# Kernel optimization log

Hardware: AMD Instinct MI355X
Metric: run time of the kernel (lower is better)

Reference implementation:

```python
import jax, jax.numpy as jnp
import numpy as np

DIM = 192
NUM_HEADS = 6
KSZ = 7
MLP_RATIO = 4.0
LEVELS = 8
EPS = 1e-5


def layernorm(x, w, b):
    mu = jnp.mean(x, axis=-1, keepdims=True)
    var = jnp.mean(jnp.square(x - mu), axis=-1, keepdims=True)
    return (x - mu) * jax.lax.rsqrt(var + EPS) * w + b


def na2d(x, qkv_w, qkv_b, proj_w, proj_b, rpb):
    # Neighborhood attention 2D with relative position bias (NATTEN semantics:
    # window of KSZ x KSZ keys per query, clamped to stay inside the image).
    B, H, W, C = x.shape
    nh, hd = NUM_HEADS, C // NUM_HEADS
    scale = hd ** -0.5
    qkv = (x @ qkv_w.T + qkv_b).reshape(B, H, W, 3, nh, hd)
    q = qkv[..., 0, :, :] * scale  # [B,H,W,nh,hd]
    k = qkv[..., 1, :, :]
    v = qkv[..., 2, :, :]

    si = jnp.clip(jnp.arange(H) - KSZ // 2, 0, H - KSZ)
    idx_i = si[:, None] + jnp.arange(KSZ)  # [H,KSZ] row indices of each window
    sj = jnp.clip(jnp.arange(W) - KSZ // 2, 0, W - KSZ)
    idx_j = sj[:, None] + jnp.arange(KSZ)  # [W,KSZ]

    def gather_win(t):  # [B,H,W,nh,hd] -> [B,H,KSZ,W,KSZ,nh,hd]
        t = jnp.take(t, idx_i.reshape(-1), axis=1).reshape(B, H, KSZ, W, nh, hd)
        t = jnp.take(t, idx_j.reshape(-1), axis=3).reshape(B, H, KSZ, W, KSZ, nh, hd)
        return t

    kw = gather_win(k)
    vw = gather_win(v)

    # scores over the KSZ x KSZ neighborhood
    scores = jnp.einsum('bxynd,bxiyjnd->bxynij', q, kw)  # [B,H,W,nh,KSZ,KSZ]

    # relative position bias: rpb is [nh, 2K-1, 2K-1]
    rel_i = idx_i - jnp.arange(H)[:, None] + (KSZ - 1)  # [H,KSZ] in [0,2K-2]
    rel_j = idx_j - jnp.arange(W)[:, None] + (KSZ - 1)  # [W,KSZ]
    bias = rpb[:, rel_i][:, :, :, rel_j]  # [nh,H,KSZ,W,KSZ]
    scores = scores + bias.transpose(1, 3, 0, 2, 4)[None]

    attn = jax.nn.softmax(scores.reshape(B, H, W, nh, KSZ * KSZ), axis=-1)
    attn = attn.reshape(B, H, W, nh, KSZ, KSZ)
    out = jnp.einsum('bxynij,bxiyjnd->bxynd', attn, vw).reshape(B, H, W, C)
    return out @ proj_w.T + proj_b


def setup_inputs() -> dict:
    key = jax.random.key(0)
    ks = jax.random.split(key, 8)
    C = DIM
    hidden = int(C * MLP_RATIO)
    init = lambda k, shape: (jax.random.normal(k, shape, dtype=jnp.float32) * 0.02)
    return {
        'x': jax.random.normal(ks[0], (1, 128, 128, C), dtype=jnp.float32),
        'qkv_w': init(ks[1], (3 * C, C)),
        'qkv_b': jnp.zeros((3 * C,), jnp.float32),
        'proj_w': init(ks[2], (C, C)),
        'proj_b': jnp.zeros((C,), jnp.float32),
        'rpb': init(ks[3], (NUM_HEADS, 2 * KSZ - 1, 2 * KSZ - 1)),
        'ln1_w': jnp.ones((C,), jnp.float32),
        'ln1_b': jnp.zeros((C,), jnp.float32),
        'ln2_w': jnp.ones((C,), jnp.float32),
        'ln2_b': jnp.zeros((C,), jnp.float32),
        'fc1_w': init(ks[4], (hidden, C)),
        'fc1_b': jnp.zeros((hidden,), jnp.float32),
        'fc2_w': init(ks[5], (C, hidden)),
        'fc2_b': jnp.zeros((C,), jnp.float32),
        'gamma1': jnp.ones((LEVELS, C), jnp.float32),
        'gamma2': jnp.ones((LEVELS, C), jnp.float32),
        'quality': 4,
    }


def reference(x, qkv_w, qkv_b, proj_w, proj_b, rpb, ln1_w, ln1_b, ln2_w, ln2_b,
              fc1_w, fc1_b, fc2_w, fc2_b, gamma1, gamma2, quality):
    # eval-mode quality gating; quality is an integer so l = quality % 1 == 0
    s = int(quality) - 1
    g1 = jnp.abs(gamma1[s])
    g2 = jnp.abs(gamma2[s])

    shortcut = x
    h = layernorm(x, ln1_w, ln1_b)
    a = na2d(h, qkv_w, qkv_b, proj_w, proj_b, rpb)
    x = shortcut + g1 * a
    h2 = layernorm(x, ln2_w, ln2_b)
    m = jax.nn.gelu(h2 @ fc1_w.T + fc1_b, approximate=False) @ fc2_w.T + fc2_b
    x = x + g2 * m
    return x
```

## Files before the change

### kernel.cpp

```cpp
#include <hip/hip_runtime.h>
#include <hip/hip_bf16.h>
#include <math.h>

#define DIM 192
#define NHD 6
#define HD 32
#define KSZ 7
#define HID 768
#define IMH 128
#define IMW 128
#define NPIX (IMH*IMW)
#define WIN 14
#define KPAD 40

typedef __attribute__((ext_vector_type(8))) short short8;
typedef __attribute__((ext_vector_type(4))) float f32x4;

__global__ __launch_bounds__(256) void cvt_ln1(
    const float* __restrict__ qw, const float* __restrict__ pw,
    const float* __restrict__ f1, const float* __restrict__ f2,
    __hip_bfloat16* dq, __hip_bfloat16* dp, __hip_bfloat16* df1, __hip_bfloat16* df2,
    const float* __restrict__ x, const float* __restrict__ w, const float* __restrict__ b,
    __hip_bfloat16* __restrict__ hout)
{
    int blk = blockIdx.x, t = threadIdx.x;
    if (blk < 432) {
        const float* s; __hip_bfloat16* d; int base;
        if (blk < 108)      { s = qw; d = dq;  base = blk * 1024; }
        else if (blk < 144) { s = pw; d = dp;  base = (blk - 108) * 1024; }
        else if (blk < 288) { s = f1; d = df1; base = (blk - 144) * 1024; }
        else                { s = f2; d = df2; base = (blk - 288) * 1024; }
        int idx = base + t * 4;
        float4 v4 = *(const float4*)(s + idx);
        union { ushort4 u; __hip_bfloat16 h[4]; } o;
        o.h[0] = __float2bfloat16(v4.x); o.h[1] = __float2bfloat16(v4.y);
        o.h[2] = __float2bfloat16(v4.z); o.h[3] = __float2bfloat16(v4.w);
        *(ushort4*)&d[idx] = o.u;
        return;
    }
    int wid  = ((blk - 432) * 256 + t) >> 6;
    int lane = t & 63;
    const float* xp = x + (size_t)wid * DIM;
    float v0 = xp[lane], v1 = xp[lane + 64], v2 = xp[lane + 128];
    float s = v0 + v1 + v2;
    #pragma unroll
    for (int off = 32; off > 0; off >>= 1) s += __shfl_down(s, off);
    float mu = __shfl(s, 0) * (1.0f / DIM);
    float d0 = v0 - mu, d1 = v1 - mu, d2 = v2 - mu;
    float q = d0*d0 + d1*d1 + d2*d2;
    #pragma unroll
    for (int off = 32; off > 0; off >>= 1) q += __shfl_down(q, off);
    float rstd = rsqrtf(__shfl(q, 0) * (1.0f / DIM) + 1e-5f);
    __hip_bfloat16* op = hout + (size_t)wid * DIM;
    op[lane]       = __float2bfloat16(d0 * rstd * w[lane]       + b[lane]);
    op[lane + 64]  = __float2bfloat16(d1 * rstd * w[lane + 64]  + b[lane + 64]);
    op[lane + 128] = __float2bfloat16(d2 * rstd * w[lane + 128] + b[lane + 128]);
}

__device__ __forceinline__ void gl_lds16(const void* g, void* l) {
    __builtin_amdgcn_global_load_lds(
        (const __attribute__((address_space(1))) void*)g,
        (__attribute__((address_space(3))) void*)l, 16, 0, 0);
}

__global__ __launch_bounds__(256) void qkv_gemm(
    const __hip_bfloat16* __restrict__ A, const __hip_bfloat16* __restrict__ W,
    const float* __restrict__ bias,
    float* __restrict__ qb, __hip_bfloat16* __restrict__ kb, __hip_bfloat16* __restrict__ vb)
{
    __shared__ __hip_bfloat16 As[128 * 192];
    __shared__ __hip_bfloat16 Bs[64 * 192];
    int tid = threadIdx.x;
    int wave = tid >> 6, lane = tid & 63;
    int m0 = blockIdx.x * 128, n0 = blockIdx.y * 64;
    int q = lane >> 4, col = lane & 15;
    int wm = (wave >> 1) * 64, wn = (wave & 1) * 32;

    const __hip_bfloat16* Ab = A + (size_t)m0 * 192;
    #pragma unroll
    for (int i = 0; i < 12; i++) {
        int c = i * 256 + tid;
        int r = c / 24, kc = c - r * 24;
        int g = kc ^ (r & 7);
        gl_lds16(Ab + r * 192 + g * 8, (char*)As + (i * 256 + wave * 64) * 16);
    }
    const __hip_bfloat16* Wb = W + (size_t)n0 * 192;
    #pragma unroll
    for (int i = 0; i < 6; i++) {
        int c = i * 256 + tid;
        int r = c / 24, kc = c - r * 24;
        int g = kc ^ (r & 7);
        gl_lds16(Wb + r * 192 + g * 8, (char*)Bs + (i * 256 + wave * 64) * 16);
    }
    __syncthreads();

    f32x4 acc[4][2] = {};
    #pragma unroll
    for (int ks = 0; ks < 6; ks++) {
        short8 af[4], bf[2];
        #pragma unroll
        for (int mi = 0; mi < 4; mi++) {
            int r = wm + mi * 16 + col;
            af[mi] = *(const short8*)&As[r * 192 + (((ks * 4 + q) ^ (r & 7)) * 8)];
        }
        #pragma unroll
        for (int ni = 0; ni < 2; ni++) {
            int r = wn + ni * 16 + col;
            bf[ni] = *(const short8*)&Bs[r * 192 + (((ks * 4 + q) ^ (r & 7)) * 8)];
        }
        #pragma unroll
        for (int mi = 0; mi < 4; mi++)
            #pragma unroll
            for (int ni = 0; ni < 2; ni++)
                acc[mi][ni] = __builtin_amdgcn_mfma_f32_16x16x32_bf16(
                    af[mi], bf[ni], acc[mi][ni], 0, 0, 0);
    }

    #pragma unroll
    for (int mi = 0; mi < 4; mi++) {
        #pragma unroll
        for (int r = 0; r < 4; r++) {
            int m = m0 + wm + mi * 16 + q * 4 + r;
            #pragma unroll
            for (int ni = 0; ni < 2; ni++) {
                int n = n0 + wn + ni * 16 + col;
                float v = acc[mi][ni][r] + bias[n];
                int h18 = n >> 5;
                int sel = h18 / 6;
                int head = h18 - sel * 6;
                size_t idx = ((size_t)head * NPIX + m) * 32 + (n & 31);
                if (sel == 0)      qb[idx] = v * 0.17677669529663687f;
                else if (sel == 1) kb[idx] = __float2bfloat16(v);
                else               vb[idx] = __float2bfloat16(v);
            }
        }
    }
}

__global__ __launch_bounds__(512, 2) void tail_fused(
    const __hip_bfloat16* __restrict__ A, const __hip_bfloat16* __restrict__ Wp,
    const float* __restrict__ pb, const float* __restrict__ resid,
    const float* __restrict__ gamma1, const float* __restrict__ ln2w, const float* __restrict__ ln2b,
    const __hip_bfloat16* __restrict__ W1, const float* __restrict__ b1,
    const __hip_bfloat16* __restrict__ W2, const float* __restrict__ b2,
    const float* __restrict__ gamma2, const int* __restrict__ quality,
    float* __restrict__ outf)
{
    __shared__ __hip_bfloat16 arena[64 * 768];
    __shared__ __hip_bfloat16 Wsb[2][64 * 192];
    __shared__ float lnred[2][64][2];
    __hip_bfloat16* Bsp = arena;
    __hip_bfloat16* Hs  = arena + 192 * 192;

    int tid = threadIdx.x;
    int wave = tid >> 6, lane = tid & 63;
    int q = lane >> 4, col = lane & 15;
    int wm = (wave >> 1) * 16, wh = wave & 1;
    int m0 = blockIdx.x * 64;

    const __hip_bfloat16* Ab = A + (size_t)m0 * DIM;
    #pragma unroll
    for (int i = 0; i < 3; i++) {
        int c = i * 512 + tid;
        int r = c / 24, kc = c - r * 24;
        gl_lds16(Ab + r * DIM + (kc ^ (r & 7)) * 8, (char*)Hs + (i * 512 + wave * 64) * 16);
    }
    #pragma unroll
    for (int i = 0; i < 9; i++) {
        int c = i * 512 + tid;
        int r = c / 24, kc = c - r * 24;
        gl_lds16(Wp + (size_t)r * DIM + (kc ^ (r & 7)) * 8, (char*)Bsp + (i * 512 + wave * 64) * 16);
    }
    __syncthreads();

    f32x4 acc[6] = {};
    #pragma unroll
    for (int ks = 0; ks < 6; ks++) {
        int rA = wm + col;
        short8 af = *(const short8*)&Hs[rA * DIM + (((ks * 4 + q) ^ (rA & 7)) * 8)];
        #pragma unroll
        for (int f = 0; f < 6; f++) {
            int rB = wh * 96 + f * 16 + col;
            short8 bf = *(const short8*)&Bsp[rB * DIM + (((ks * 4 + q) ^ (rB & 7)) * 8)];
            acc[f] = __builtin_amdgcn_mfma_f32_16x16x32_bf16(af, bf, acc[f], 0, 0, 0);
        }
    }

    int s = quality[0] - 1;
    float v[6][4];
    float sm[4] = {}, sq[4] = {};
    #pragma unroll
    for (int f = 0; f < 6; f++) {
        int n = wh * 96 + f * 16 + col;
        float bi = pb[n];
        float g = fabsf(gamma1[s * DIM + n]);
        #pragma unroll
        for (int r = 0; r < 4; r++) {
            int m = m0 + wm + q * 4 + r;
            v[f][r] = resid[(size_t)m * DIM + n] + g * (acc[f][r] + bi);
            sm[r] += v[f][r]; sq[r] += v[f][r] * v[f][r];
        }
    }
    #pragma unroll
    for (int off = 1; off <= 8; off <<= 1)
        #pragma unroll
        for (int r = 0; r < 4; r++) {
            sm[r] += __shfl_xor(sm[r], off);
            sq[r] += __shfl_xor(sq[r], off);
        }
    if (col == 0) {
        #pragma unroll
        for (int r = 0; r < 4; r++) {
            lnred[wh][wm + q * 4 + r][0] = sm[r];
            lnred[wh][wm + q * 4 + r][1] = sq[r];
        }
    }
    __syncthreads();
    float mu[4], rstd[4];
    #pragma unroll
    for (int r = 0; r < 4; r++) {
        int ml = wm + q * 4 + r;
        float smt = lnred[0][ml][0] + lnred[1][ml][0];
        float sqt = lnred[0][ml][1] + lnred[1][ml][1];
        mu[r] = smt * (1.0f / DIM);
        float var = sqt * (1.0f / DIM) - mu[r] * mu[r];
        rstd[r] = rsqrtf(var + 1e-5f);
    }
    #pragma unroll
    for (int f = 0; f < 6; f++) {
        int n = wh * 96 + f * 16 + col;
        float lw = ln2w[n], lb = ln2b[n];
        #pragma unroll
        for (int r = 0; r < 4; r++) {
            int ml = wm + q * 4 + r;
            Hs[ml * DIM + (((n >> 3) ^ (ml & 7)) * 8) + (n & 7)] =
                __float2bfloat16((v[f][r] - mu[r]) * rstd[r] * lw + lb);
        }
    }
    __syncthreads();
    short8 af1[6];
    {
        int rowA = wm + col;
        #pragma unroll
        for (int ks = 0; ks < 6; ks++)
            af1[ks] = *(const short8*)&Hs[rowA * DIM + (((ks * 4 + q) ^ (rowA & 7)) * 8)];
    }
    __syncthreads();

    auto stage1 = [&](int t, int buf) {
        #pragma unroll
        for (int i = 0; i < 3; i++) {
            int c = i * 512 + tid;
            int r = c / 24, kc = c - r * 24;
            gl_lds16(W1 + (size_t)(t * 64 + r) * DIM + (kc ^ (r & 7)) * 8,
                     (char*)&Wsb[buf][0] + (i * 512 + wave * 64) * 16);
        }
    };
    auto stage2 = [&](int ch, int buf) {
        #pragma unroll
        for (int i = 0; i < 3; i++) {
            int idx = i * 512 + tid;
            int r = idx >> 3, o = idx & 7;
            gl_lds16(W2 + (size_t)r * HID + ch * 64 + ((o ^ (r & 7)) * 8),
                     (char*)&Wsb[buf][0] + (i * 512 + wave * 64) * 16);
        }
    };
    __hip_bfloat16* Ms = arena;

    stage1(0, 0);
    for (int t = 0; t < 12; t++) {
        if (t < 11) stage1(t + 1, (t + 1) & 1);
        else        stage2(0, 0);
        asm volatile("s_waitcnt vmcnt(3)" ::: "memory");
        __builtin_amdgcn_s_barrier();
        const __hip_bfloat16* wsb = &Wsb[t & 1][0];
        f32x4 a1[2] = {};
        #pragma unroll
        for (int ks = 0; ks < 6; ks++) {
            #pragma unroll
            for (int ni = 0; ni < 2; ni++) {
                int r = wh * 32 + ni * 16 + col;
                short8 bf = *(const short8*)&wsb[r * DIM + (((ks * 4 + q) ^ (r & 7)) * 8)];
                a1[ni] = __builtin_amdgcn_mfma_f32_16x16x32_bf16(af1[ks], bf, a1[ni], 0, 0, 0);
            }
        }
        #pragma unroll
        for (int ni = 0; ni < 2; ni++) {
            int n = t * 64 + wh * 32 + ni * 16 + col;
            float bi = b1[n];
            int oct = n >> 3;
            #pragma unroll
            for (int r4 = 0; r4 < 4; r4++) {
                int row = wm + q * 4 + r4;
                float vv = a1[ni][r4] + bi;
                float u = 0.7978845608f * (vv + 0.044715f * vv * vv * vv);
                float tt = 1.f - 2.f / (__expf(2.f * u) + 1.f);
                vv = 0.5f * vv * (1.f + tt);
                int osw = (oct & ~7) | ((oct ^ row) & 7);
                *(__hip_bfloat16*)((char*)Ms + row * 1536 + osw * 16 + (n & 7) * 2) =
                    __float2bfloat16(vv);
            }
        }
        __builtin_amdgcn_s_barrier();
    }
    __syncthreads();

    int wn2 = wh * 96;
    f32x4 acc2[6] = {};
    for (int ch = 0; ch < 12; ch++) {
        stage2(ch < 11 ? ch + 1 : 11, (ch + 1) & 1);
        asm volatile("s_waitcnt vmcnt(3)" ::: "memory");
        __builtin_amdgcn_s_barrier();
        const __hip_bfloat16* wsb = &Wsb[ch & 1][0];
        #pragma unroll
        for (int ks = 0; ks < 2; ks++) {
            int row = wm + col;
            int og = ch * 8 + ks * 4 + q;
            int osw = (og & ~7) | ((og ^ row) & 7);
            short8 a2 = *(const short8*)((char*)Ms + row * 1536 + osw * 16);
            #pragma unroll
            for (int f = 0; f < 6; f++) {
                int r = wn2 + f * 16 + col;
                short8 bf = *(const short8*)&wsb[r * 64 + (((ks * 4 + q) ^ (r & 7)) * 8)];
                acc2[f] = __builtin_amdgcn_mfma_f32_16x16x32_bf16(a2, bf, acc2[f], 0, 0, 0);
            }
        }
        __builtin_amdgcn_s_barrier();
    }
    #pragma unroll
    for (int f = 0; f < 6; f++) {
        int n = wn2 + f * 16 + col;
        float g = fabsf(gamma2[s * DIM + n]);
        float bi = b2[n];
        #pragma unroll
        for (int r4 = 0; r4 < 4; r4++) {
            int m = m0 + wm + q * 4 + r4;
            outf[(size_t)m * DIM + n] = v[f][r4] + g * (acc2[f][r4] + bi);
        }
    }
}

__device__ __forceinline__ void unpack8(const __hip_bfloat16* ptr, float* f) {
    short8 s8 = *(const short8*)ptr;
    union { short8 v; unsigned u[4]; } c; c.v = s8;
    #pragma unroll
    for (int w = 0; w < 4; w++) {
        f[2*w]   = __uint_as_float(c.u[w] << 16);
        f[2*w+1] = __uint_as_float(c.u[w] & 0xffff0000u);
    }
}

__global__ __launch_bounds__(256, 4) void attn_kernel3(
    const float* __restrict__ qbuf, const __hip_bfloat16* __restrict__ kbuf,
    const __hip_bfloat16* __restrict__ vbuf, const float* __restrict__ rpb,
    __hip_bfloat16* __restrict__ out)
{
    __shared__ __hip_bfloat16 Ks[WIN * WIN * KPAD];
    __shared__ __hip_bfloat16 Vs[WIN * WIN * KPAD];
    __shared__ float rpbs[169];

    int head = blockIdx.y;
    int tile = blockIdx.x;
    int ti0 = (tile >> 4) * 8;
    int tj0 = (tile & 15) * 8;
    int wi0 = ti0 - 3; wi0 = wi0 < 0 ? 0 : (wi0 > IMH - WIN ? IMH - WIN : wi0);
    int wj0 = tj0 - 3; wj0 = wj0 < 0 ? 0 : (wj0 > IMW - WIN ? IMW - WIN : wj0);

    int tid = threadIdx.x;
    const size_t hbase = (size_t)head * NPIX;

    for (int c = tid; c < 784; c += 256) {
        int i = c / 56, part = c - i * 56;
        int n = i * WIN + (part >> 2);
        int dp = part & 3;
        size_t goff = (hbase + (size_t)(wi0 + i) * IMW + wj0) * 32 + part * 8;
        short8 kk = *(const short8*)(kbuf + goff);
        short8 vv = *(const short8*)(vbuf + goff);
        *(short8*)&Ks[n * KPAD + dp * 8] = kk;
        *(short8*)&Vs[n * KPAD + dp * 8] = vv;
    }
    if (tid < 169) rpbs[tid] = rpb[head * 169 + tid];

    int p   = tid >> 2;
    int sub = tid & 3;
    int pi = ti0 + (p >> 3), pj = tj0 + (p & 7);
    int si = pi - 3; si = si < 0 ? 0 : (si > IMH - KSZ ? IMH - KSZ : si);
    int sj = pj - 3; sj = sj < 0 ? 0 : (sj > IMW - KSZ ? IMW - KSZ : sj);
    int bi = si - wi0, bj = sj - wj0;

    const float4* qp = (const float4*)(qbuf + (hbase + (size_t)(pi * IMW + pj)) * 32 + sub * 8);
    float4 q0 = qp[0], q1 = qp[1];
    float q[8] = {q0.x, q0.y, q0.z, q0.w, q1.x, q1.y, q1.z, q1.w};

    __syncthreads();

    float m = -1e30f, l = 0.f;
    float acc[8] = {};
    #pragma unroll
    for (int ki = 0; ki < KSZ; ki++) {
        int rbase = (bi + ki) * WIN + bj;
        const float* rb = &rpbs[(si + ki - pi + 6) * 13 + (sj - pj + 6)];
        float s7[KSZ];
        #pragma unroll
        for (int kj = 0; kj < KSZ; kj++) {
            float kf[8];
            unpack8(&Ks[(rbase + kj) * KPAD + sub * 8], kf);
            float d = q[0]*kf[0] + q[1]*kf[1] + q[2]*kf[2] + q[3]*kf[3]
                    + q[4]*kf[4] + q[5]*kf[5] + q[6]*kf[6] + q[7]*kf[7];
            d += __shfl_xor(d, 1);
            d += __shfl_xor(d, 2);
            s7[kj] = d + rb[kj];
        }
        float rmax = s7[0];
        #pragma unroll
        for (int kj = 1; kj < KSZ; kj++) rmax = fmaxf(rmax, s7[kj]);
        float mn = fmaxf(m, rmax);
        float co = __expf(m - mn);
        l *= co;
        #pragma unroll
        for (int e = 0; e < 8; e++) acc[e] *= co;
        #pragma unroll
        for (int kj = 0; kj < KSZ; kj++) {
            float pw = __expf(s7[kj] - mn);
            l += pw;
            float vf[8];
            unpack8(&Vs[(rbase + kj) * KPAD + sub * 8], vf);
            #pragma unroll
            for (int e = 0; e < 8; e++) acc[e] += pw * vf[e];
        }
        m = mn;
    }
    float rl = 1.f / l;
    __hip_bfloat16* op = out + (size_t)(pi * IMW + pj) * DIM + head * HD + sub * 8;
    #pragma unroll
    for (int e = 0; e < 8; e++) op[e] = __float2bfloat16(acc[e] * rl);
}

extern "C" void kernel_launch(void* const* d_in, const int* in_sizes, int n_in,
                              void* d_out, int out_size, void* d_ws, size_t ws_size,
                              hipStream_t stream)
{
    const float* x      = (const float*)d_in[0];
    const float* qkv_w  = (const float*)d_in[1];
    const float* qkv_b  = (const float*)d_in[2];
    const float* proj_w = (const float*)d_in[3];
    const float* proj_b = (const float*)d_in[4];
    const float* rpb    = (const float*)d_in[5];
    const float* ln1_w  = (const float*)d_in[6];
    const float* ln1_b  = (const float*)d_in[7];
    const float* ln2_w  = (const float*)d_in[8];
    const float* ln2_b  = (const float*)d_in[9];
    const float* fc1_w  = (const float*)d_in[10];
    const float* fc1_b  = (const float*)d_in[11];
    const float* fc2_w  = (const float*)d_in[12];
    const float* fc2_b  = (const float*)d_in[13];
    const float* gamma1 = (const float*)d_in[14];
    const float* gamma2 = (const float*)d_in[15];
    const int*   quality= (const int*)d_in[16];
    float* out = (float*)d_out;

    char* ws = (char*)d_ws;
    float*          qbuf   = (float*)ws;
    __hip_bfloat16* kbuf   = (__hip_bfloat16*)(ws + 12582912);
    __hip_bfloat16* vbuf   = (__hip_bfloat16*)(ws + 18874368);
    __hip_bfloat16* h      = (__hip_bfloat16*)(ws + 37748736);
    __hip_bfloat16* attn_b = (__hip_bfloat16*)(ws + 44040192);
    __hip_bfloat16* wq     = (__hip_bfloat16*)(ws + 50331648);
    __hip_bfloat16* wp     = (__hip_bfloat16*)(ws + 50552832);
    __hip_bfloat16* wf1    = (__hip_bfloat16*)(ws + 50626560);
    __hip_bfloat16* wf2    = (__hip_bfloat16*)(ws + 50921472);

    cvt_ln1<<<432 + NPIX / 4, 256, 0, stream>>>(
        qkv_w, proj_w, fc1_w, fc2_w, wq, wp, wf1, wf2, x, ln1_w, ln1_b, h);
    qkv_gemm<<<dim3(NPIX / 128, 9), 256, 0, stream>>>(
        h, wq, qkv_b, qbuf, kbuf, vbuf);
    attn_kernel3<<<dim3(256, NHD), 256, 0, stream>>>(qbuf, kbuf, vbuf, rpb, attn_b);
    tail_fused<<<256, 512, 0, stream>>>(
        attn_b, wp, proj_b, x, gamma1, ln2_w, ln2_b,
        wf1, fc1_b, wf2, fc2_b, gamma2, quality, out);
}
```

Baseline: 175.9 us.

## Fuse LayerNorm1 into QKV GEMM with double-buffered weight chunk streaming

LayerNorm1 moves out of the weight-conversion kernel and into the QKV GEMM. Each block normalizes a 32-row tile of x straight into LDS as bf16, then loops over nine 64-column weight chunks with double-buffered async global-to-LDS loads. This removes the bf16 h round trip through global memory and one launch's worth of work. In exchange each block re-streams the full QKV weight, and the small 32-row tile gives less MFMA reuse per weight load.

```diff
diff --git a/kernel.cpp b/kernel.cpp
--- a/kernel.cpp
+++ b/kernel.cpp
@@ -16,45 +16,23 @@
 typedef __attribute__((ext_vector_type(8))) short short8;
 typedef __attribute__((ext_vector_type(4))) float f32x4;
 
-__global__ __launch_bounds__(256) void cvt_ln1(
+__global__ __launch_bounds__(256) void cvt_w(
     const float* __restrict__ qw, const float* __restrict__ pw,
     const float* __restrict__ f1, const float* __restrict__ f2,
-    __hip_bfloat16* dq, __hip_bfloat16* dp, __hip_bfloat16* df1, __hip_bfloat16* df2,
-    const float* __restrict__ x, const float* __restrict__ w, const float* __restrict__ b,
-    __hip_bfloat16* __restrict__ hout)
+    __hip_bfloat16* dq, __hip_bfloat16* dp, __hip_bfloat16* df1, __hip_bfloat16* df2)
 {
     int blk = blockIdx.x, t = threadIdx.x;
-    if (blk < 432) {
-        const float* s; __hip_bfloat16* d; int base;
-        if (blk < 108)      { s = qw; d = dq;  base = blk * 1024; }
-        else if (blk < 144) { s = pw; d = dp;  base = (blk - 108) * 1024; }
-        else if (blk < 288) { s = f1; d = df1; base = (blk - 144) * 1024; }
-        else                { s = f2; d = df2; base = (blk - 288) * 1024; }
-        int idx = base + t * 4;
-        float4 v4 = *(const float4*)(s + idx);
-        union { ushort4 u; __hip_bfloat16 h[4]; } o;
-        o.h[0] = __float2bfloat16(v4.x); o.h[1] = __float2bfloat16(v4.y);
-        o.h[2] = __float2bfloat16(v4.z); o.h[3] = __float2bfloat16(v4.w);
-        *(ushort4*)&d[idx] = o.u;
-        return;
-    }
-    int wid  = ((blk - 432) * 256 + t) >> 6;
-    int lane = t & 63;
-    const float* xp = x + (size_t)wid * DIM;
-    float v0 = xp[lane], v1 = xp[lane + 64], v2 = xp[lane + 128];
-    float s = v0 + v1 + v2;
-    #pragma unroll
-    for (int off = 32; off > 0; off >>= 1) s += __shfl_down(s, off);
-    float mu = __shfl(s, 0) * (1.0f / DIM);
-    float d0 = v0 - mu, d1 = v1 - mu, d2 = v2 - mu;
-    float q = d0*d0 + d1*d1 + d2*d2;
-    #pragma unroll
-    for (int off = 32; off > 0; off >>= 1) q += __shfl_down(q, off);
-    float rstd = rsqrtf(__shfl(q, 0) * (1.0f / DIM) + 1e-5f);
-    __hip_bfloat16* op = hout + (size_t)wid * DIM;
-    op[lane]       = __float2bfloat16(d0 * rstd * w[lane]       + b[lane]);
-    op[lane + 64]  = __float2bfloat16(d1 * rstd * w[lane + 64]  + b[lane + 64]);
-    op[lane + 128] = __float2bfloat16(d2 * rstd * w[lane + 128] + b[lane + 128]);
+    const float* s; __hip_bfloat16* d; int base;
+    if (blk < 108)      { s = qw; d = dq;  base = blk * 1024; }
+    else if (blk < 144) { s = pw; d = dp;  base = (blk - 108) * 1024; }
+    else if (blk < 288) { s = f1; d = df1; base = (blk - 144) * 1024; }
+    else                { s = f2; d = df2; base = (blk - 288) * 1024; }
+    int idx = base + t * 4;
+    float4 v4 = *(const float4*)(s + idx);
+    union { ushort4 u; __hip_bfloat16 h[4]; } o;
+    o.h[0] = __float2bfloat16(v4.x); o.h[1] = __float2bfloat16(v4.y);
+    o.h[2] = __float2bfloat16(v4.z); o.h[3] = __float2bfloat16(v4.w);
+    *(ushort4*)&d[idx] = o.u;
 }
 
 __device__ __forceinline__ void gl_lds16(const void* g, void* l) {
@@ -63,77 +41,128 @@
         (__attribute__((address_space(3))) void*)l, 16, 0, 0);
 }
 
-__global__ __launch_bounds__(256) void qkv_gemm(
-    const __hip_bfloat16* __restrict__ A, const __hip_bfloat16* __restrict__ W,
-    const float* __restrict__ bias,
+__device__ __forceinline__ short8 cvt8(float4 a, float4 b) {
+    union { short8 v; __hip_bfloat16 h[8]; } u;
+    u.h[0] = __float2bfloat16(a.x); u.h[1] = __float2bfloat16(a.y);
+    u.h[2] = __float2bfloat16(a.z); u.h[3] = __float2bfloat16(a.w);
+    u.h[4] = __float2bfloat16(b.x); u.h[5] = __float2bfloat16(b.y);
+    u.h[6] = __float2bfloat16(b.z); u.h[7] = __float2bfloat16(b.w);
+    return u.v;
+}
+
+__global__ __launch_bounds__(256, 2) void qkv_ln_gemm(
+    const float* __restrict__ x, const float* __restrict__ lnw, const float* __restrict__ lnb,
+    const __hip_bfloat16* __restrict__ W, const float* __restrict__ bias,
     float* __restrict__ qb, __hip_bfloat16* __restrict__ kb, __hip_bfloat16* __restrict__ vb)
 {
-    __shared__ __hip_bfloat16 As[128 * 192];
-    __shared__ __hip_bfloat16 Bs[64 * 192];
+    __shared__ __hip_bfloat16 As[32 * 192];
+    __shared__ __hip_bfloat16 Ws2[2][64 * 192];
     int tid = threadIdx.x;
     int wave = tid >> 6, lane = tid & 63;
-    int m0 = blockIdx.x * 128, n0 = blockIdx.y * 64;
     int q = lane >> 4, col = lane & 15;
-    int wm = (wave >> 1) * 64, wn = (wave & 1) * 32;
-
-    const __hip_bfloat16* Ab = A + (size_t)m0 * 192;
-    #pragma unroll
-    for (int i = 0; i < 12; i++) {
-        int c = i * 256 + tid;
-        int r = c / 24, kc = c - r * 24;
-        int g = kc ^ (r & 7);
-        gl_lds16(Ab + r * 192 + g * 8, (char*)As + (i * 256 + wave * 64) * 16);
-    }
-    const __hip_bfloat16* Wb = W + (size_t)n0 * 192;
-    #pragma unroll
-    for (int i = 0; i < 6; i++) {
-        int c = i * 256 + tid;
-        int r = c / 24, kc = c - r * 24;
-        int g = kc ^ (r & 7);
-        gl_lds16(Wb + r * 192 + g * 8, (char*)Bs + (i * 256 + wave * 64) * 16);
-    }
-    __syncthreads();
-
-    f32x4 acc[4][2] = {};
-    #pragma unroll
-    for (int ks = 0; ks < 6; ks++) {
-        short8 af[4], bf[2];
-        #pragma unroll
-        for (int mi = 0; mi < 4; mi++) {
-            int r = wm + mi * 16 + col;
-            af[mi] = *(const short8*)&As[r * 192 + (((ks * 4 + q) ^ (r & 7)) * 8)];
-        }
-        #pragma unroll
-        for (int ni = 0; ni < 2; ni++) {
-            int r = wn + ni * 16 + col;
-            bf[ni] = *(const short8*)&Bs[r * 192 + (((ks * 4 + q) ^ (r & 7)) * 8)];
-        }
-        #pragma unroll
-        for (int mi = 0; mi < 4; mi++)
-            #pragma unroll
-            for (int ni = 0; ni < 2; ni++)
-                acc[mi][ni] = __builtin_amdgcn_mfma_f32_16x16x32_bf16(
-                    af[mi], bf[ni], acc[mi][ni], 0, 0, 0);
-    }
-
-    #pragma unroll
-    for (int mi = 0; mi < 4; mi++) {
-        #pragma unroll
-        for (int r = 0; r < 4; r++) {
-            int m = m0 + wm + mi * 16 + q * 4 + r;
+    int wm = (wave >> 1) * 16, wn = (wave & 1) * 32;
+    int m0 = blockIdx.x * 32;
+
+    auto stageW = [&](int ch, int buf) {
+        #pragma unroll
+        for (int i = 0; i < 6; i++) {
+            int c = i * 256 + tid;
+            int r = c / 24, kc = c - r * 24;
+            gl_lds16(W + (size_t)(ch * 64 + r) * DIM + ((kc ^ (r & 7)) * 8),
+                     (char*)&Ws2[buf][0] + (i * 256 + wave * 64) * 16);
+        }
+    };
+
+    stageW(0, 0);
+
+    {
+        int row = tid >> 3, sub = tid & 7;
+        const float4* xr = (const float4*)(x + (size_t)(m0 + row) * DIM + sub * 24);
+        float4 xa[6];
+        float s = 0.f;
+        #pragma unroll
+        for (int i = 0; i < 6; i++) {
+            xa[i] = xr[i];
+            s += xa[i].x + xa[i].y + xa[i].z + xa[i].w;
+        }
+        s += __shfl_xor(s, 1); s += __shfl_xor(s, 2); s += __shfl_xor(s, 4);
+        float mu = s * (1.0f / DIM);
+        float qs = 0.f;
+        #pragma unroll
+        for (int i = 0; i < 6; i++) {
+            float a = xa[i].x - mu, b = xa[i].y - mu, c = xa[i].z - mu, d = xa[i].w - mu;
+            qs += a * a + b * b + c * c + d * d;
+        }
+        qs += __shfl_xor(qs, 1); qs += __shfl_xor(qs, 2); qs += __shfl_xor(qs, 4);
+        float rstd = rsqrtf(qs * (1.0f / DIM) + 1e-5f);
+        const float4* wv = (const float4*)(lnw + sub * 24);
+        const float4* bv = (const float4*)(lnb + sub * 24);
+        #pragma unroll
+        for (int j = 0; j < 3; j++) {
+            float4 v0 = xa[j * 2], v1 = xa[j * 2 + 1];
+            float4 w0 = wv[j * 2], w1 = wv[j * 2 + 1];
+            float4 b0 = bv[j * 2], b1 = bv[j * 2 + 1];
+            float4 o0, o1;
+            o0.x = (v0.x - mu) * rstd * w0.x + b0.x;
+            o0.y = (v0.y - mu) * rstd * w0.y + b0.y;
+            o0.z = (v0.z - mu) * rstd * w0.z + b0.z;
+            o0.w = (v0.w - mu) * rstd * w0.w + b0.w;
+            o1.x = (v1.x - mu) * rstd * w1.x + b1.x;
+            o1.y = (v1.y - mu) * rstd * w1.y + b1.y;
+            o1.z = (v1.z - mu) * rstd * w1.z + b1.z;
+            o1.w = (v1.w - mu) * rstd * w1.w + b1.w;
+            int oct = sub * 3 + j;
+            *(short8*)&As[row * 192 + ((oct ^ (row & 7)) * 8)] = cvt8(o0, o1);
+        }
+    }
+    asm volatile("s_waitcnt lgkmcnt(0)" ::: "memory");
+    __builtin_amdgcn_s_barrier();
+
+    short8 af[6];
+    {
+        int rA = wm + col;
+        #pragma unroll
+        for (int ks = 0; ks < 6; ks++)
+            af[ks] = *(const short8*)&As[rA * 192 + (((ks * 4 + q) ^ (rA & 7)) * 8)];
+    }
+
+    for (int ch = 0; ch < 9; ch++) {
+        if (ch < 8) {
+            stageW(ch + 1, (ch + 1) & 1);
+            asm volatile("s_waitcnt vmcnt(6)" ::: "memory");
+        } else {
+            asm volatile("s_waitcnt vmcnt(0)" ::: "memory");
+        }
+        __builtin_amdgcn_s_barrier();
+        const __hip_bfloat16* wsb = &Ws2[ch & 1][0];
+        f32x4 acc[2] = {};
+        #pragma unroll
+        for (int ks = 0; ks < 6; ks++) {
             #pragma unroll
             for (int ni = 0; ni < 2; ni++) {
-                int n = n0 + wn + ni * 16 + col;
-                float v = acc[mi][ni][r] + bias[n];
-                int h18 = n >> 5;
-                int sel = h18 / 6;
-                int head = h18 - sel * 6;
+                int rB = wn + ni * 16 + col;
+                short8 bf = *(const short8*)&wsb[rB * 192 + (((ks * 4 + q) ^ (rB & 7)) * 8)];
+                acc[ni] = __builtin_amdgcn_mfma_f32_16x16x32_bf16(af[ks], bf, acc[ni], 0, 0, 0);
+            }
+        }
+        #pragma unroll
+        for (int ni = 0; ni < 2; ni++) {
+            int n = ch * 64 + wn + ni * 16 + col;
+            float bi = bias[n];
+            int h18 = n >> 5;
+            int sel = h18 / 6;
+            int head = h18 - sel * 6;
+            #pragma unroll
+            for (int r4 = 0; r4 < 4; r4++) {
+                int m = m0 + wm + q * 4 + r4;
+                float v = acc[ni][r4] + bi;
                 size_t idx = ((size_t)head * NPIX + m) * 32 + (n & 31);
                 if (sel == 0)      qb[idx] = v * 0.17677669529663687f;
                 else if (sel == 1) kb[idx] = __float2bfloat16(v);
                 else               vb[idx] = __float2bfloat16(v);
             }
         }
+        __builtin_amdgcn_s_barrier();
     }
 }
 
@@ -463,17 +492,15 @@
     float*          qbuf   = (float*)ws;
     __hip_bfloat16* kbuf   = (__hip_bfloat16*)(ws + 12582912);
     __hip_bfloat16* vbuf   = (__hip_bfloat16*)(ws + 18874368);
-    __hip_bfloat16* h      = (__hip_bfloat16*)(ws + 37748736);
     __hip_bfloat16* attn_b = (__hip_bfloat16*)(ws + 44040192);
     __hip_bfloat16* wq     = (__hip_bfloat16*)(ws + 50331648);
     __hip_bfloat16* wp     = (__hip_bfloat16*)(ws + 50552832);
     __hip_bfloat16* wf1    = (__hip_bfloat16*)(ws + 50626560);
     __hip_bfloat16* wf2    = (__hip_bfloat16*)(ws + 50921472);
 
-    cvt_ln1<<<432 + NPIX / 4, 256, 0, stream>>>(
-        qkv_w, proj_w, fc1_w, fc2_w, wq, wp, wf1, wf2, x, ln1_w, ln1_b, h);
-    qkv_gemm<<<dim3(NPIX / 128, 9), 256, 0, stream>>>(
-        h, wq, qkv_b, qbuf, kbuf, vbuf);
+    cvt_w<<<432, 256, 0, stream>>>(qkv_w, proj_w, fc1_w, fc2_w, wq, wp, wf1, wf2);
+    qkv_ln_gemm<<<512, 256, 0, stream>>>(
+        x, ln1_w, ln1_b, wq, qkv_b, qbuf, kbuf, vbuf);
     attn_kernel3<<<dim3(256, NHD), 256, 0, stream>>>(qbuf, kbuf, vbuf, rpb, attn_b);
     tail_fused<<<256, 512, 0, stream>>>(
         attn_b, wp, proj_b, x, gamma1, ln2_w, ln2_b,
```

Result: faster. 170.7 us (-3.0%).
